# Performance work log

Measured on AMD Instinct MI355X. Metric: run time of the kernel, lower is better.

The kernel has to match this reference:

```python
import jax, jax.numpy as jnp
import numpy as np

K = 5          # k = min(5, min(S, T)) with S = T = 4096
SIGMA = 1.0
EPS_VAR = 1e-08
EPS_LOG = 1e-08


def _entropy(p):
    # sum(-p * log2(clamp(p, 1e-8)), axis=1).mean()
    return jnp.sum(-p * jnp.log2(jnp.clip(p, EPS_LOG, None)), axis=1).mean()


def _pairwise_dist(x):
    # Euclidean cdist via GEMM (matches torch's use_mm_for_euclid path)
    sq = jnp.sum(x * x, axis=1)                       # [N]
    d2 = sq[:, None] + sq[None, :] - 2.0 * (x @ x.T)  # [N, N]
    d2 = jnp.maximum(d2, 0.0)
    # safe sqrt (zero diagonal) — value identical, grad-safe
    return jnp.where(d2 > 0, jnp.sqrt(jnp.where(d2 > 0, d2, 1.0)), 0.0)


def _row_var(block):
    # sqrt(k-th smallest distance per row + eps): max of k smallest
    kth = -jax.lax.top_k(-block, K)[0][:, -1]
    return jnp.sqrt(kth + EPS_VAR)                    # [rows]


def _sim(block, var_row, zero_diag):
    s = jnp.exp(-block / (2.0 * (var_row[:, None] * SIGMA) ** 2))
    if zero_diag:
        n = block.shape[0]
        s = s * (1.0 - jnp.eye(n, dtype=s.dtype))
    return s


def _forward(Feature_all, logit_all, y_source):
    S = y_source.shape[0]
    logit_source = logit_all[:S]
    logit_target = logit_all[S:]

    # cross-entropy on source
    logp = jax.nn.log_softmax(logit_source, axis=1)
    loss_cl = -jnp.take_along_axis(logp, y_source[:, None], axis=1).mean()

    # entropy of target softmax
    loss_ce = _entropy(jax.nn.softmax(logit_target, axis=1))

    # reg_loss_dist
    dist = _pairwise_dist(Feature_all)                # [N, N]
    d_ss = dist[:S, :S]
    d_st = dist[:S, S:]
    d_tt = dist[S:, S:]
    d_ts = dist[S:, :S]

    sim_ss = _sim(d_ss, _row_var(d_ss), True)
    sim_st = _sim(d_st, _row_var(d_st), False)
    sim_tt = _sim(d_tt, _row_var(d_tt), True)
    sim_ts = _sim(d_ts, _row_var(d_ts), False)

    src_intra = jnp.max(sim_ss, axis=1)
    src_inter = jnp.max(sim_st, axis=1)
    tgt_intra = jnp.max(sim_tt, axis=1)
    tgt_inter = jnp.max(sim_ts, axis=1)

    loss_reg = (jnp.abs(src_intra - src_inter).mean()
                + jnp.abs(tgt_intra - tgt_inter).mean())
    return loss_cl, loss_ce, loss_reg


def setup_inputs() -> dict:
    key = jax.random.key(0)
    k1, k2, k3 = jax.random.split(key, 3)
    N, D, C, S = 8192, 256, 65, 4096
    return {
        "Feature_all": jax.random.normal(k1, (N, D), dtype=jnp.float32),
        "logit_all": jax.random.normal(k2, (N, C), dtype=jnp.float32),
        "y_source": jax.random.randint(k3, (S,), 0, C, dtype=jnp.int64
                                       if jax.config.jax_enable_x64 else jnp.int32),
        "device": 0,
    }


def reference(Feature_all, logit_all, y_source, device):
    del device  # torch-specific, ignored
    return _forward(Feature_all, logit_all, y_source)
```

## Files before the change

### kernel.cpp

```cpp
#include <hip/hip_runtime.h>
#include <stdint.h>

#define Nn 8192
#define Dd 256
#define Ss 4096
#define Cc 65

#define TI 128
#define TJ 128
#define BK 32
#define CHUNK 1024
#define NCHUNK (Nn / CHUNK)
#define NJT (CHUNK / TJ)
#define KS (Dd / BK)

#define BIGF 3.0e37f

typedef float f4 __attribute__((ext_vector_type(4)));
typedef __bf16 bf8 __attribute__((ext_vector_type(8)));

__device__ __forceinline__ float wredsum(float v) {
#pragma unroll
  for (int o = 32; o; o >>= 1) v += __shfl_xor(v, o, 64);
  return v;
}
__device__ __forceinline__ float wredmax(float v) {
#pragma unroll
  for (int o = 32; o; o >>= 1) v = fmaxf(v, __shfl_xor(v, o, 64));
  return v;
}

__device__ __forceinline__ unsigned short f2bf(float f) {
  unsigned int u = __float_as_uint(f);
  u = (u + 0x7fffu + ((u >> 16) & 1u)) >> 16;
  return (unsigned short)u;
}

__device__ __forceinline__ void merge5(const float* a, const float* b, float* o) {
  o[0] = fminf(a[0], b[0]);
  o[1] = fminf(fminf(a[1], b[1]), fmaxf(a[0], b[0]));
  o[2] = fminf(fminf(a[2], b[2]), fminf(fmaxf(a[1], b[0]), fmaxf(a[0], b[1])));
  o[3] = fminf(fminf(a[3], b[3]), fminf(fmaxf(a[2], b[0]), fminf(fmaxf(a[1], b[1]), fmaxf(a[0], b[2]))));
  o[4] = fminf(fminf(a[4], b[4]),
               fminf(fmaxf(a[3], b[0]),
                     fminf(fmaxf(a[2], b[1]), fminf(fmaxf(a[1], b[2]), fmaxf(a[0], b[3])))));
}

__global__ __launch_bounds__(256) void prep_loss_kernel(const float* __restrict__ X,
                                                        unsigned short* __restrict__ xb,
                                                        float* __restrict__ sqn,
                                                        const float* __restrict__ logit,
                                                        const int* __restrict__ y,
                                                        float* __restrict__ part_cl,
                                                        float* __restrict__ part_ce,
                                                        unsigned int* __restrict__ counter) {
  if (blockIdx.x == 0 && threadIdx.x == 0) *counter = 0u;
  int lane = threadIdx.x & 63;
  if (blockIdx.x < 2048) {
    int row = blockIdx.x * 4 + (threadIdx.x >> 6);
    f4 v = ((const f4*)(X + (size_t)row * Dd))[lane];
    float ss = v[0] * v[0] + v[1] * v[1] + v[2] * v[2] + v[3] * v[3];
    ss = wredsum(ss);
    if (lane == 0) sqn[row] = ss;
    ushort4 o;
    o.x = f2bf(v[0]); o.y = f2bf(v[1]); o.z = f2bf(v[2]); o.w = f2bf(v[3]);
    ((ushort4*)(xb + (size_t)row * Dd))[lane] = o;
  } else {
    int bid = blockIdx.x - 2048;
    int row = bid * 4 + (threadIdx.x >> 6);
    const float* xr = logit + (size_t)row * Cc;
    float x1 = xr[lane];
    float x2 = (lane == 0) ? xr[64] : -BIGF;
    float mx = wredmax(fmaxf(x1, x2));
    float e1 = expf(x1 - mx);
    float e2 = (lane == 0) ? expf(x2 - mx) : 0.f;
    float Z = wredsum(e1 + e2);
    float res;
    if (row < Ss) {
      int yy = y[row];
      float pick = (lane == yy ? x1 : 0.f) + ((lane == 0 && yy == 64) ? x2 : 0.f);
      float xy = wredsum(pick);
      res = -(xy - mx - logf(Z));
    } else {
      float p1 = e1 / Z;
      float t1 = -p1 * log2f(fmaxf(p1, 1e-8f));
      if (lane == 0) {
        float p2 = e2 / Z;
        t1 += -p2 * log2f(fmaxf(p2, 1e-8f));
      }
      res = wredsum(t1);
    }
    __shared__ float a4[4];
    if (lane == 0) a4[threadIdx.x >> 6] = res;
    __syncthreads();
    if (threadIdx.x == 0) {
      float s = a4[0] + a4[1] + a4[2] + a4[3];
      if (bid < 1024) part_cl[bid] = s;
      else part_ce[bid - 1024] = s;
    }
  }
}

__device__ __forceinline__ void stage16(const void* g, void* l) {
  __builtin_amdgcn_global_load_lds((__attribute__((address_space(1))) void*)g,
                                   (__attribute__((address_space(3))) void*)l, 16, 0, 0);
}

__global__ __launch_bounds__(512, 4) void dist_kernel(const unsigned short* __restrict__ xb,
                                                      const float* __restrict__ sqn,
                                                      float* __restrict__ top5ws) {
  __shared__ unsigned short ldsA[2][TJ * BK];
  __shared__ unsigned short ldsBf[KS][TI * BK];

  const int tid = threadIdx.x;
  const int lane = tid & 63;
  const int wv = tid >> 6;
  const int q = lane >> 4;
  const int c = lane & 15;
  const int jw = wv & 1;
  const int iq = wv >> 1;

  const int ib = (blockIdx.x / NCHUNK) * TI;
  const int chunk = blockIdx.x % NCHUNK;
  const int jc0 = chunk * CHUNK;

  const int swz = q ^ ((lane >> 1) & 3);
  const int pr = lane >> 2;
  const int qd = (lane & 3) ^ ((lane >> 3) & 3);
  const int gcol = qd * 8;

  float top[2][5];
#pragma unroll
  for (int a = 0; a < 2; ++a)
#pragma unroll
    for (int b = 0; b < 5; ++b) top[a][b] = BIGF;

  const int iwbase = ib + iq * 32;

#pragma unroll
  for (int ks = 0; ks < KS; ++ks)
    stage16(xb + (size_t)(ib + wv * 16 + pr) * Dd + ks * BK + gcol, &ldsBf[ks][wv * 512]);

  for (int jt = 0; jt < NJT; ++jt) {
    const int jb = jc0 + jt * TJ;

    f4 acc[4][2];
    f4 z = {0.f, 0.f, 0.f, 0.f};
#pragma unroll
    for (int a = 0; a < 4; ++a)
#pragma unroll
      for (int b2 = 0; b2 < 2; ++b2) acc[a][b2] = z;

    stage16(xb + (size_t)(jb + wv * 16 + pr) * Dd + gcol, &ldsA[0][wv * 512]);
    __syncthreads();

#pragma unroll
    for (int ks = 0; ks < KS; ++ks) {
      const int b = ks & 1;
      if (ks + 1 < KS)
        stage16(xb + (size_t)(jb + wv * 16 + pr) * Dd + (ks + 1) * BK + gcol,
                &ldsA[b ^ 1][wv * 512]);
      bf8 aF[4], bF[2];
#pragma unroll
      for (int rt = 0; rt < 4; ++rt)
        aF[rt] = *(const bf8*)&ldsA[b][(jw * 64 + rt * 16 + c) * 32 + swz * 8];
#pragma unroll
      for (int ct = 0; ct < 2; ++ct)
        bF[ct] = *(const bf8*)&ldsBf[ks][(iq * 32 + ct * 16 + c) * 32 + swz * 8];
#pragma unroll
      for (int rt = 0; rt < 4; ++rt)
#pragma unroll
        for (int ct = 0; ct < 2; ++ct)
          acc[rt][ct] = __builtin_amdgcn_mfma_f32_16x16x32_bf16(aF[rt], bF[ct], acc[rt][ct], 0, 0, 0);
      __syncthreads();
    }

    const int jrow = jb + jw * 64;
    f4 sq4[4];
#pragma unroll
    for (int rt = 0; rt < 4; ++rt) sq4[rt] = *(const f4*)&sqn[jrow + rt * 16 + q * 4];
    const bool mayDiag = (jb == ib) && ((iq >> 1) == jw);
#pragma unroll
    for (int ct = 0; ct < 2; ++ct) {
      float t[16];
#pragma unroll
      for (int rt = 0; rt < 4; ++rt)
#pragma unroll
        for (int r = 0; r < 4; ++r)
          t[rt * 4 + r] = fmaf(acc[rt][ct][r], -2.0f, sq4[rt][r]);
      if (mayDiag && ((c >> 2) == q))
        t[((iq & 1) * 2 + ct) * 4 + (c & 3)] = BIGF;
      float tm = fminf(fminf(fminf(fminf(t[0], t[1]), fminf(t[2], t[3])),
                             fminf(fminf(t[4], t[5]), fminf(t[6], t[7]))),
                       fminf(fminf(fminf(t[8], t[9]), fminf(t[10], t[11])),
                             fminf(fminf(t[12], t[13]), fminf(t[14], t[15]))));
      if (tm < top[ct][4]) {
#pragma unroll
        for (int kk = 0; kk < 16; ++kk) {
          float x = t[kk];
          if (x < top[ct][4]) {
#pragma unroll
            for (int s = 0; s < 4; ++s) {
              float lo = fminf(top[ct][s], x);
              x = fmaxf(top[ct][s], x);
              top[ct][s] = lo;
            }
            top[ct][4] = x;
          }
        }
      }
    }
  }

  float fin[2][5];
#pragma unroll
  for (int ct = 0; ct < 2; ++ct) {
    float a0 = top[ct][0], a1 = top[ct][1], a2 = top[ct][2], a3 = top[ct][3], a4 = top[ct][4];
#pragma unroll
    for (int off = 16; off <= 32; off <<= 1) {
      float b0 = __shfl_xor(a0, off, 64);
      float b1 = __shfl_xor(a1, off, 64);
      float b2 = __shfl_xor(a2, off, 64);
      float b3 = __shfl_xor(a3, off, 64);
      float b4 = __shfl_xor(a4, off, 64);
      float c0 = fminf(a0, b0);
      float c1 = fminf(fminf(a1, b1), fmaxf(a0, b0));
      float c2 = fminf(fminf(a2, b2), fminf(fmaxf(a1, b0), fmaxf(a0, b1)));
      float c3 = fminf(fminf(a3, b3), fminf(fmaxf(a2, b0), fminf(fmaxf(a1, b1), fmaxf(a0, b2))));
      float c4 = fminf(fminf(a4, b4),
                       fminf(fmaxf(a3, b0),
                             fminf(fmaxf(a2, b1), fminf(fmaxf(a1, b2), fmaxf(a0, b3)))));
      a0 = c0; a1 = c1; a2 = c2; a3 = c3; a4 = c4;
    }
    fin[ct][0] = a0; fin[ct][1] = a1; fin[ct][2] = a2; fin[ct][3] = a3; fin[ct][4] = a4;
  }

  float* mbuf = (float*)ldsA;
  if (jw == 1 && q == 0) {
#pragma unroll
    for (int ct = 0; ct < 2; ++ct) {
      float* m = mbuf + ((((iq << 1) | ct) << 4) + c) * 5;
      m[0] = fin[ct][0]; m[1] = fin[ct][1]; m[2] = fin[ct][2]; m[3] = fin[ct][3]; m[4] = fin[ct][4];
    }
  }
  __syncthreads();
  if (jw == 0 && q == 0) {
#pragma unroll
    for (int ct = 0; ct < 2; ++ct) {
      const float* m = mbuf + ((((iq << 1) | ct) << 4) + c) * 5;
      float bl[5] = {m[0], m[1], m[2], m[3], m[4]};
      float o[5];
      merge5(fin[ct], bl, o);
      int i = iwbase + ct * 16 + c;
      float* dst = top5ws + ((size_t)i * NCHUNK + chunk) * 5;
      dst[0] = o[0]; dst[1] = o[1]; dst[2] = o[2]; dst[3] = o[3]; dst[4] = o[4];
    }
  }
}

__device__ __forceinline__ void merge4lists(const float* L, float* o) {
  float m01[5], m23[5];
  merge5(L + 0, L + 5, m01);
  merge5(L + 10, L + 15, m23);
  merge5(m01, m23, o);
}

__global__ __launch_bounds__(256) void reg_final_kernel(const float* __restrict__ top5ws,
                                                        const float* __restrict__ sqn,
                                                        float* __restrict__ part_reg,
                                                        const float* __restrict__ part_cl,
                                                        const float* __restrict__ part_ce,
                                                        float* __restrict__ out,
                                                        unsigned int* __restrict__ counter) {
  int i = blockIdx.x * 256 + threadIdx.x;
  float buf[40];
  const float* L = top5ws + (size_t)i * 40;
#pragma unroll
  for (int k = 0; k < 40; ++k) buf[k] = L[k];
  float mlo[5], mhi[5];
  merge4lists(buf, mlo);
  merge4lists(buf + 20, mhi);
  bool srcRow = (i < Ss);
  float A0 = srcRow ? mlo[0] : mhi[0];
  float A3 = srcRow ? mlo[3] : mhi[3];
  float B0 = srcRow ? mhi[0] : mlo[0];
  float B4 = srcRow ? mhi[4] : mlo[4];
  float sq = sqn[i];
  float dmin_a = sqrtf(fmaxf(A0 + sq, 0.f));
  float kth_a = sqrtf(fmaxf(A3 + sq, 0.f));
  float dmin_b = sqrtf(fmaxf(B0 + sq, 0.f));
  float kth_b = sqrtf(fmaxf(B4 + sq, 0.f));
  float sa = expf(-dmin_a / (2.f * (kth_a + 1e-8f)));
  float sb = expf(-dmin_b / (2.f * (kth_b + 1e-8f)));
  float v = fabsf(sa - sb);
  __shared__ float red[256];
  red[threadIdx.x] = v;
  __syncthreads();
#pragma unroll
  for (int s = 128; s; s >>= 1) {
    if (threadIdx.x < s) red[threadIdx.x] += red[threadIdx.x + s];
    __syncthreads();
  }
  if (threadIdx.x == 0) part_reg[blockIdx.x] = red[0];

  __shared__ unsigned int lastFlag;
  __threadfence();
  if (threadIdx.x == 0) lastFlag = (atomicAdd(counter, 1u) == 31u) ? 1u : 0u;
  __syncthreads();
  if (!lastFlag) return;
  __threadfence();

  __shared__ double dred[256];
  int tid = threadIdx.x;
  double a = 0.0;
  for (int k = tid; k < 1024; k += 256) a += (double)part_cl[k];
  dred[tid] = a; __syncthreads();
  for (int s = 128; s; s >>= 1) { if (tid < s) dred[tid] += dred[tid + s]; __syncthreads(); }
  double cl = dred[0]; __syncthreads();
  a = 0.0;
  for (int k = tid; k < 1024; k += 256) a += (double)part_ce[k];
  dred[tid] = a; __syncthreads();
  for (int s = 128; s; s >>= 1) { if (tid < s) dred[tid] += dred[tid + s]; __syncthreads(); }
  double ce = dred[0]; __syncthreads();
  a = (tid < 16) ? (double)part_reg[tid] : 0.0;
  dred[tid] = a; __syncthreads();
  for (int s = 128; s; s >>= 1) { if (tid < s) dred[tid] += dred[tid + s]; __syncthreads(); }
  double rs = dred[0]; __syncthreads();
  a = (tid >= 16 && tid < 32) ? (double)part_reg[tid] : 0.0;
  dred[tid] = a; __syncthreads();
  for (int s = 128; s; s >>= 1) { if (tid < s) dred[tid] += dred[tid + s]; __syncthreads(); }
  if (tid == 0) {
    out[0] = (float)(cl / 4096.0);
    out[1] = (float)(ce / 4096.0);
    out[2] = (float)(rs / 4096.0 + dred[0] / 4096.0);
  }
}

extern "C" void kernel_launch(void* const* d_in, const int* in_sizes, int n_in,
                              void* d_out, int out_size, void* d_ws, size_t ws_size,
                              hipStream_t stream) {
  (void)in_sizes; (void)n_in; (void)out_size; (void)ws_size;
  const float* X = (const float*)d_in[0];
  const float* logit = (const float*)d_in[1];
  const int* y = (const int*)d_in[2];
  float* out = (float*)d_out;
  char* ws = (char*)d_ws;

  unsigned short* xb = (unsigned short*)ws;
  float* sqn = (float*)(ws + (4u << 20));
  float* top5 = (float*)(ws + (4u << 20) + (64u << 10));
  float* part_cl = (float*)(ws + (7u << 20));
  float* part_ce = part_cl + 1024;
  float* part_reg = part_ce + 1024;
  unsigned int* counter = (unsigned int*)(part_reg + 32);

  hipLaunchKernelGGL(prep_loss_kernel, dim3(4096), dim3(256), 0, stream, X, xb, sqn, logit, y,
                     part_cl, part_ce, counter);
  hipLaunchKernelGGL(dist_kernel, dim3((Nn / TI) * NCHUNK), dim3(512), 0, stream, xb, sqn, top5);
  hipLaunchKernelGGL(reg_final_kernel, dim3(32), dim3(256), 0, stream, top5, sqn, part_reg,
                     part_cl, part_ce, out, counter);
}
```

Baseline: 141.4 us.

## Exploit distance-matrix symmetry to compute only upper-triangle tile pairs

Replaces the full N×N distance GEMM with a symmetric scheme. Each block takes a row tile and a set of cyclic offset column tiles, covering about half of the tile pairs. It updates top-5 lists for both the row side (in LDS) and the column side (through a transposed LDS buffer and shuffle merges), writing per-slot lists to a larger workspace. The final kernel merges 48 slots per row instead of 8. This roughly halves the MFMA work, at the cost of extra transpose, sync and top-5 merge overhead, less B-tile reuse (the I tile is now re-staged each tile), and only 512 blocks.

```diff
diff --git a/kernel.cpp b/kernel.cpp
--- a/kernel.cpp
+++ b/kernel.cpp
@@ -6,13 +6,11 @@
 #define Ss 4096
 #define Cc 65
 
-#define TI 128
-#define TJ 128
+#define TT 128
+#define NTILE 64
 #define BK 32
-#define CHUNK 1024
-#define NCHUNK (Nn / CHUNK)
-#define NJT (CHUNK / TJ)
 #define KS (Dd / BK)
+#define NSLOT 48
 
 #define BIGF 3.0e37f
 
@@ -44,6 +42,45 @@
   o[4] = fminf(fminf(a[4], b[4]),
                fminf(fmaxf(a[3], b[0]),
                      fminf(fmaxf(a[2], b[1]), fminf(fmaxf(a[1], b[2]), fmaxf(a[0], b[3])))));
+}
+
+__device__ __forceinline__ void mshfl5(float (&a)[5], int off) {
+  float b0 = __shfl_xor(a[0], off, 64);
+  float b1 = __shfl_xor(a[1], off, 64);
+  float b2 = __shfl_xor(a[2], off, 64);
+  float b3 = __shfl_xor(a[3], off, 64);
+  float b4 = __shfl_xor(a[4], off, 64);
+  float c0 = fminf(a[0], b0);
+  float c1 = fminf(fminf(a[1], b1), fmaxf(a[0], b0));
+  float c2 = fminf(fminf(a[2], b2), fminf(fmaxf(a[1], b0), fmaxf(a[0], b1)));
+  float c3 = fminf(fminf(a[3], b3), fminf(fmaxf(a[2], b0), fminf(fmaxf(a[1], b1), fmaxf(a[0], b2))));
+  float c4 = fminf(fminf(a[4], b4),
+                   fminf(fmaxf(a[3], b0),
+                         fminf(fmaxf(a[2], b1), fminf(fmaxf(a[1], b2), fmaxf(a[0], b3)))));
+  a[0] = c0; a[1] = c1; a[2] = c2; a[3] = c3; a[4] = c4;
+}
+
+__device__ __forceinline__ void ins5(float x, float (&tp)[5]) {
+  if (x < tp[4]) {
+#pragma unroll
+    for (int s2 = 0; s2 < 4; ++s2) {
+      float lo = fminf(tp[s2], x);
+      x = fmaxf(tp[s2], x);
+      tp[s2] = lo;
+    }
+    tp[4] = x;
+  }
+}
+
+__device__ __forceinline__ void instile16(const float* tv, float (&tp)[5]) {
+  float tm = fminf(fminf(fminf(fminf(tv[0], tv[1]), fminf(tv[2], tv[3])),
+                         fminf(fminf(tv[4], tv[5]), fminf(tv[6], tv[7]))),
+                   fminf(fminf(fminf(tv[8], tv[9]), fminf(tv[10], tv[11])),
+                         fminf(fminf(tv[12], tv[13]), fminf(tv[14], tv[15]))));
+  if (tm < tp[4]) {
+#pragma unroll
+    for (int kk = 0; kk < 16; ++kk) ins5(tv[kk], tp);
+  }
 }
 
 __global__ __launch_bounds__(256) void prep_loss_kernel(const float* __restrict__ X,
@@ -106,43 +143,53 @@
                                    (__attribute__((address_space(3))) void*)l, 16, 0, 0);
 }
 
-__global__ __launch_bounds__(512, 4) void dist_kernel(const unsigned short* __restrict__ xb,
-                                                      const float* __restrict__ sqn,
-                                                      float* __restrict__ top5ws) {
-  __shared__ unsigned short ldsA[2][TJ * BK];
-  __shared__ unsigned short ldsBf[KS][TI * BK];
+__global__ __launch_bounds__(512, 4) void dist_sym_kernel(const unsigned short* __restrict__ xb,
+                                                          const float* __restrict__ sqn,
+                                                          float* __restrict__ top5ws) {
+  __shared__ unsigned short ldsMem[2][2][TT * BK];
+  __shared__ float iLists[TT * 2 * 5];
 
   const int tid = threadIdx.x;
   const int lane = tid & 63;
   const int wv = tid >> 6;
   const int q = lane >> 4;
   const int c = lane & 15;
+  const int l16 = lane >> 4;
   const int jw = wv & 1;
   const int iq = wv >> 1;
 
-  const int ib = (blockIdx.x / NCHUNK) * TI;
-  const int chunk = blockIdx.x % NCHUNK;
-  const int jc0 = chunk * CHUNK;
+  const int I = blockIdx.x >> 3;
+  const int s = blockIdx.x & 7;
+  const int Ibase = I * TT;
 
   const int swz = q ^ ((lane >> 1) & 3);
   const int pr = lane >> 2;
   const int qd = (lane & 3) ^ ((lane >> 3) & 3);
   const int gcol = qd * 8;
 
-  float top[2][5];
-#pragma unroll
-  for (int a = 0; a < 2; ++a)
-#pragma unroll
-    for (int b = 0; b < 5; ++b) top[a][b] = BIGF;
-
-  const int iwbase = ib + iq * 32;
-
-#pragma unroll
-  for (int ks = 0; ks < KS; ++ks)
-    stage16(xb + (size_t)(ib + wv * 16 + pr) * Dd + ks * BK + gcol, &ldsBf[ks][wv * 512]);
-
-  for (int jt = 0; jt < NJT; ++jt) {
-    const int jb = jc0 + jt * TJ;
+  const int nt = (s == 7 && I < 32) ? 5 : 4;
+
+  const float sqi0 = sqn[Ibase + iq * 32 + c];
+  const float sqi1 = sqn[Ibase + iq * 32 + 16 + c];
+
+  if (tid < 256) {
+#pragma unroll
+    for (int k = 0; k < 5; ++k) iLists[tid * 5 + k] = BIGF;
+  }
+  __syncthreads();
+
+  float* gbuf = (float*)&ldsMem[1][0][0];
+  float* scratch = (float*)&ldsMem[0][0][0];
+
+  for (int t = 0; t < nt; ++t) {
+    const int e = (t < 4) ? (s + 8 * t) : 32;
+    const int J = (I + e) & 63;
+    const int Jbase = J * TT;
+    const int half = (J >= 32) ? 1 : 0;
+
+    stage16(xb + (size_t)(Jbase + wv * 16 + pr) * Dd + gcol, &ldsMem[0][0][wv * 512]);
+    stage16(xb + (size_t)(Ibase + wv * 16 + pr) * Dd + gcol, &ldsMem[1][0][wv * 512]);
+    __syncthreads();
 
     f4 acc[4][2];
     f4 z = {0.f, 0.f, 0.f, 0.f};
@@ -151,135 +198,151 @@
 #pragma unroll
       for (int b2 = 0; b2 < 2; ++b2) acc[a][b2] = z;
 
-    stage16(xb + (size_t)(jb + wv * 16 + pr) * Dd + gcol, &ldsA[0][wv * 512]);
-    __syncthreads();
-
 #pragma unroll
     for (int ks = 0; ks < KS; ++ks) {
       const int b = ks & 1;
-      if (ks + 1 < KS)
-        stage16(xb + (size_t)(jb + wv * 16 + pr) * Dd + (ks + 1) * BK + gcol,
-                &ldsA[b ^ 1][wv * 512]);
-      bf8 aF[4], bF[2];
+      if (ks + 1 < KS) {
+        const int k0 = (ks + 1) * BK;
+        stage16(xb + (size_t)(Jbase + wv * 16 + pr) * Dd + k0 + gcol, &ldsMem[0][b ^ 1][wv * 512]);
+        stage16(xb + (size_t)(Ibase + wv * 16 + pr) * Dd + k0 + gcol, &ldsMem[1][b ^ 1][wv * 512]);
+      }
+      bf8 aF[4], bF2[2];
 #pragma unroll
       for (int rt = 0; rt < 4; ++rt)
-        aF[rt] = *(const bf8*)&ldsA[b][(jw * 64 + rt * 16 + c) * 32 + swz * 8];
+        aF[rt] = *(const bf8*)&ldsMem[0][b][(jw * 64 + rt * 16 + c) * 32 + swz * 8];
 #pragma unroll
       for (int ct = 0; ct < 2; ++ct)
-        bF[ct] = *(const bf8*)&ldsBf[ks][(iq * 32 + ct * 16 + c) * 32 + swz * 8];
+        bF2[ct] = *(const bf8*)&ldsMem[1][b][(iq * 32 + ct * 16 + c) * 32 + swz * 8];
 #pragma unroll
       for (int rt = 0; rt < 4; ++rt)
 #pragma unroll
         for (int ct = 0; ct < 2; ++ct)
-          acc[rt][ct] = __builtin_amdgcn_mfma_f32_16x16x32_bf16(aF[rt], bF[ct], acc[rt][ct], 0, 0, 0);
+          acc[rt][ct] = __builtin_amdgcn_mfma_f32_16x16x32_bf16(aF[rt], bF2[ct], acc[rt][ct], 0, 0, 0);
       __syncthreads();
     }
 
-    const int jrow = jb + jw * 64;
+    const int jrow = Jbase + jw * 64;
     f4 sq4[4];
 #pragma unroll
     for (int rt = 0; rt < 4; ++rt) sq4[rt] = *(const f4*)&sqn[jrow + rt * 16 + q * 4];
-    const bool mayDiag = (jb == ib) && ((iq >> 1) == jw);
+    const bool mayDiag = (e == 0) && ((iq >> 1) == jw);
+    float tloc[2][5];
+#pragma unroll
+    for (int a = 0; a < 2; ++a)
+#pragma unroll
+      for (int b2 = 0; b2 < 5; ++b2) tloc[a][b2] = BIGF;
 #pragma unroll
     for (int ct = 0; ct < 2; ++ct) {
-      float t[16];
+      float tv[16];
 #pragma unroll
       for (int rt = 0; rt < 4; ++rt)
 #pragma unroll
         for (int r = 0; r < 4; ++r)
-          t[rt * 4 + r] = fmaf(acc[rt][ct][r], -2.0f, sq4[rt][r]);
+          tv[rt * 4 + r] = fmaf(acc[rt][ct][r], -2.0f, sq4[rt][r]);
       if (mayDiag && ((c >> 2) == q))
-        t[((iq & 1) * 2 + ct) * 4 + (c & 3)] = BIGF;
-      float tm = fminf(fminf(fminf(fminf(t[0], t[1]), fminf(t[2], t[3])),
-                             fminf(fminf(t[4], t[5]), fminf(t[6], t[7]))),
-                       fminf(fminf(fminf(t[8], t[9]), fminf(t[10], t[11])),
-                             fminf(fminf(t[12], t[13]), fminf(t[14], t[15]))));
-      if (tm < top[ct][4]) {
-#pragma unroll
-        for (int kk = 0; kk < 16; ++kk) {
-          float x = t[kk];
-          if (x < top[ct][4]) {
-#pragma unroll
-            for (int s = 0; s < 4; ++s) {
-              float lo = fminf(top[ct][s], x);
-              x = fmaxf(top[ct][s], x);
-              top[ct][s] = lo;
-            }
-            top[ct][4] = x;
+        tv[((iq & 1) * 2 + ct) * 4 + (c & 3)] = BIGF;
+      instile16(tv, tloc[ct]);
+      mshfl5(tloc[ct], 16);
+      mshfl5(tloc[ct], 32);
+    }
+    if (jw == 1 && q == 0) {
+#pragma unroll
+      for (int ct = 0; ct < 2; ++ct) {
+        float* m = &scratch[(iq * 32 + ct * 16 + c) * 5];
+        m[0] = tloc[ct][0]; m[1] = tloc[ct][1]; m[2] = tloc[ct][2];
+        m[3] = tloc[ct][3]; m[4] = tloc[ct][4];
+      }
+    }
+    __syncthreads();
+    if (jw == 0 && q == 0) {
+#pragma unroll
+      for (int ct = 0; ct < 2; ++ct) {
+        const int iloc = iq * 32 + ct * 16 + c;
+        float o1[5], o2[5];
+        merge5(tloc[ct], &scratch[iloc * 5], o1);
+        float* il = &iLists[(iloc * 2 + half) * 5];
+        merge5(o1, il, o2);
+        il[0] = o2[0]; il[1] = o2[1]; il[2] = o2[2]; il[3] = o2[3]; il[4] = o2[4];
+      }
+    }
+    __syncthreads();
+
+    if (e != 0) {
+#pragma unroll
+      for (int ss = 0; ss < 4; ++ss) {
+        if (jw == (ss >> 1)) {
+#pragma unroll
+          for (int rt2 = 0; rt2 < 2; ++rt2) {
+            const int rt = (ss & 1) * 2 + rt2;
+#pragma unroll
+            for (int ct2 = 0; ct2 < 2; ++ct2)
+#pragma unroll
+              for (int r = 0; r < 4; ++r) {
+                const int row = rt2 * 16 + q * 4 + r;
+                const int col = iq * 32 + ct2 * 16 + c;
+                const int pcol = col ^ (((row >> 2) & 1) << 4);
+                gbuf[row * 128 + pcol] = fmaf(acc[rt][ct2][r], -2.0f, ct2 ? sqi1 : sqi0);
+              }
           }
         }
+        __syncthreads();
+        const int rr = (wv & 3) | (l16 << 2) | ((wv >> 2) << 4);
+        const int Xr = ((rr >> 2) & 1) << 4;
+        f4 v0 = *(const f4*)&gbuf[rr * 128 + ((c * 4) ^ Xr)];
+        f4 v1 = *(const f4*)&gbuf[rr * 128 + ((64 + c * 4) ^ Xr)];
+        float l5[5] = {BIGF, BIGF, BIGF, BIGF, BIGF};
+        ins5(v0[0], l5); ins5(v0[1], l5); ins5(v0[2], l5); ins5(v0[3], l5);
+        ins5(v1[0], l5); ins5(v1[1], l5); ins5(v1[2], l5); ins5(v1[3], l5);
+        mshfl5(l5, 1); mshfl5(l5, 2); mshfl5(l5, 4); mshfl5(l5, 8);
+        if (c == 0) {
+          const int jg = Jbase + ss * 32 + rr;
+          float* dst = top5ws + ((size_t)jg * NSLOT + 15 + e) * 5;
+          dst[0] = l5[0]; dst[1] = l5[1]; dst[2] = l5[2]; dst[3] = l5[3]; dst[4] = l5[4];
+        }
+        __syncthreads();
       }
     }
   }
 
-  float fin[2][5];
-#pragma unroll
-  for (int ct = 0; ct < 2; ++ct) {
-    float a0 = top[ct][0], a1 = top[ct][1], a2 = top[ct][2], a3 = top[ct][3], a4 = top[ct][4];
-#pragma unroll
-    for (int off = 16; off <= 32; off <<= 1) {
-      float b0 = __shfl_xor(a0, off, 64);
-      float b1 = __shfl_xor(a1, off, 64);
-      float b2 = __shfl_xor(a2, off, 64);
-      float b3 = __shfl_xor(a3, off, 64);
-      float b4 = __shfl_xor(a4, off, 64);
-      float c0 = fminf(a0, b0);
-      float c1 = fminf(fminf(a1, b1), fmaxf(a0, b0));
-      float c2 = fminf(fminf(a2, b2), fminf(fmaxf(a1, b0), fmaxf(a0, b1)));
-      float c3 = fminf(fminf(a3, b3), fminf(fmaxf(a2, b0), fminf(fmaxf(a1, b1), fmaxf(a0, b2))));
-      float c4 = fminf(fminf(a4, b4),
-                       fminf(fmaxf(a3, b0),
-                             fminf(fmaxf(a2, b1), fminf(fmaxf(a1, b2), fmaxf(a0, b3)))));
-      a0 = c0; a1 = c1; a2 = c2; a3 = c3; a4 = c4;
-    }
-    fin[ct][0] = a0; fin[ct][1] = a1; fin[ct][2] = a2; fin[ct][3] = a3; fin[ct][4] = a4;
-  }
-
-  float* mbuf = (float*)ldsA;
-  if (jw == 1 && q == 0) {
-#pragma unroll
-    for (int ct = 0; ct < 2; ++ct) {
-      float* m = mbuf + ((((iq << 1) | ct) << 4) + c) * 5;
-      m[0] = fin[ct][0]; m[1] = fin[ct][1]; m[2] = fin[ct][2]; m[3] = fin[ct][3]; m[4] = fin[ct][4];
-    }
-  }
-  __syncthreads();
-  if (jw == 0 && q == 0) {
-#pragma unroll
-    for (int ct = 0; ct < 2; ++ct) {
-      const float* m = mbuf + ((((iq << 1) | ct) << 4) + c) * 5;
-      float bl[5] = {m[0], m[1], m[2], m[3], m[4]};
-      float o[5];
-      merge5(fin[ct], bl, o);
-      int i = iwbase + ct * 16 + c;
-      float* dst = top5ws + ((size_t)i * NCHUNK + chunk) * 5;
-      dst[0] = o[0]; dst[1] = o[1]; dst[2] = o[2]; dst[3] = o[3]; dst[4] = o[4];
-    }
-  }
-}
-
-__device__ __forceinline__ void merge4lists(const float* L, float* o) {
-  float m01[5], m23[5];
-  merge5(L + 0, L + 5, m01);
-  merge5(L + 10, L + 15, m23);
-  merge5(m01, m23, o);
-}
-
-__global__ __launch_bounds__(256) void reg_final_kernel(const float* __restrict__ top5ws,
-                                                        const float* __restrict__ sqn,
-                                                        float* __restrict__ part_reg,
-                                                        const float* __restrict__ part_cl,
-                                                        const float* __restrict__ part_ce,
-                                                        float* __restrict__ out,
-                                                        unsigned int* __restrict__ counter) {
+  if (tid < 256) {
+    const int row = tid >> 1;
+    const int h = tid & 1;
+    const float* src = &iLists[(row * 2 + h) * 5];
+    float* dst = top5ws + ((size_t)(Ibase + row) * NSLOT + (s * 2 + h)) * 5;
+    dst[0] = src[0]; dst[1] = src[1]; dst[2] = src[2]; dst[3] = src[3]; dst[4] = src[4];
+  }
+}
+
+__global__ __launch_bounds__(256) void reg_sym_kernel(const float* __restrict__ top5ws,
+                                                      const float* __restrict__ sqn,
+                                                      float* __restrict__ part_reg,
+                                                      const float* __restrict__ part_cl,
+                                                      const float* __restrict__ part_ce,
+                                                      float* __restrict__ out,
+                                                      unsigned int* __restrict__ counter) {
   int i = blockIdx.x * 256 + threadIdx.x;
-  float buf[40];
-  const float* L = top5ws + (size_t)i * 40;
-#pragma unroll
-  for (int k = 0; k < 40; ++k) buf[k] = L[k];
+  const float* L = top5ws + (size_t)i * (NSLOT * 5);
   float mlo[5], mhi[5];
-  merge4lists(buf, mlo);
-  merge4lists(buf + 20, mhi);
+#pragma unroll
+  for (int k = 0; k < 5; ++k) { mlo[k] = BIGF; mhi[k] = BIGF; }
+#pragma unroll
+  for (int sl = 0; sl < 16; ++sl) {
+    const float* p = L + sl * 5;
+    float b[5] = {p[0], p[1], p[2], p[3], p[4]};
+    float o[5];
+    if (sl & 1) { merge5(mhi, b, o); mhi[0]=o[0]; mhi[1]=o[1]; mhi[2]=o[2]; mhi[3]=o[3]; mhi[4]=o[4]; }
+    else        { merge5(mlo, b, o); mlo[0]=o[0]; mlo[1]=o[1]; mlo[2]=o[2]; mlo[3]=o[3]; mlo[4]=o[4]; }
+  }
+  const int R = i >> 7;
+  const int nd = (R >= 32) ? 32 : 31;
+  for (int d = 1; d <= nd; ++d) {
+    const float* p = L + (15 + d) * 5;
+    float b[5] = {p[0], p[1], p[2], p[3], p[4]};
+    const int It = (R - d + 64) & 63;
+    float o[5];
+    if (It >= 32) { merge5(mhi, b, o); mhi[0]=o[0]; mhi[1]=o[1]; mhi[2]=o[2]; mhi[3]=o[3]; mhi[4]=o[4]; }
+    else          { merge5(mlo, b, o); mlo[0]=o[0]; mlo[1]=o[1]; mlo[2]=o[2]; mlo[3]=o[3]; mlo[4]=o[4]; }
+  }
   bool srcRow = (i < Ss);
   float A0 = srcRow ? mlo[0] : mhi[0];
   float A3 = srcRow ? mlo[3] : mhi[3];
@@ -349,14 +412,14 @@
   unsigned short* xb = (unsigned short*)ws;
   float* sqn = (float*)(ws + (4u << 20));
   float* top5 = (float*)(ws + (4u << 20) + (64u << 10));
-  float* part_cl = (float*)(ws + (7u << 20));
+  float* part_cl = (float*)(ws + (13u << 20));
   float* part_ce = part_cl + 1024;
   float* part_reg = part_ce + 1024;
   unsigned int* counter = (unsigned int*)(part_reg + 32);
 
   hipLaunchKernelGGL(prep_loss_kernel, dim3(4096), dim3(256), 0, stream, X, xb, sqn, logit, y,
                      part_cl, part_ce, counter);
-  hipLaunchKernelGGL(dist_kernel, dim3((Nn / TI) * NCHUNK), dim3(512), 0, stream, xb, sqn, top5);
-  hipLaunchKernelGGL(reg_final_kernel, dim3(32), dim3(256), 0, stream, top5, sqn, part_reg,
+  hipLaunchKernelGGL(dist_sym_kernel, dim3(NTILE * 8), dim3(512), 0, stream, xb, sqn, top5);
+  hipLaunchKernelGGL(reg_sym_kernel, dim3(32), dim3(256), 0, stream, top5, sqn, part_reg,
                      part_cl, part_ce, out, counter);
 }
```

After: 174.8 us. 1.24x slower.
